# Optimization experiments

Measured on AMD Instinct MI355X. Metric: run time of the kernel, lower is better.

## Reference

```python
import math
import jax, jax.numpy as jnp
import numpy as np

WS = [2048, 4096, 8192]
RS = [1, 2, 4]
HEAD_IDX = 0


def build_indices(n):
    """Static dilated gather indices: concat of every segment's strided slice.

    Matches _prepare_sparse_indices for the chosen (ws, rs, n), which yields
    zero padding (each segment contributes exactly max_subatt_n indices).
    """
    max_m = min(n, max(w // r for w, r in zip(WS, RS)))
    parts = []
    for w, r in zip(WS, RS):
        offset = HEAD_IDX % r
        for s in range(0, n, w):
            seg = np.arange(s, min(s + w, n))[offset::r]
            assert len(seg) == max_m, "config chosen to avoid padding"
            parts.append(seg)
    return np.concatenate(parts).astype(np.int32), max_m


def _forward(x, Wq, Wk, Wv):
    b, n, c = x.shape
    idx_np, m = build_indices(n)
    idx = jnp.asarray(idx_np)            # [S], S = num_subatt * m
    S = idx_np.shape[0]
    nb = S // m                          # number of sub-attention windows

    # gather -> [b, S, c] -> batched windows [b*nb, m, c]
    bx = x[:, idx, :].reshape(b * nb, m, c)

    # single-head causal attention on each window, also return softmax denoms
    scale = 1.0 / math.sqrt(c)
    q = bx @ Wq
    k = bx @ Wk
    v = bx @ Wv
    logits = jnp.einsum('bqc,bkc->bqk', q, k) * scale
    causal = jnp.tril(jnp.ones((m, m), dtype=bool))
    logits = jnp.where(causal, logits, -jnp.inf)
    lse = jax.scipy.special.logsumexp(logits, axis=-1)   # [b*nb, m]
    probs = jnp.exp(logits - lse[..., None])
    o = jnp.einsum('bqk,bkc->bqc', probs, v)             # [b*nb, m, c]
    denoms = jnp.exp(lse)                                 # softmax denominators

    o = o.reshape(b, S, c)
    denoms = denoms.reshape(b, S)

    # _mix_outputs: scatter-add denoms per target position, reweight, scatter-add outputs
    denom_sums = jnp.zeros((b, n), x.dtype).at[:, idx].add(denoms)
    alphas = denoms / denom_sums[:, idx]                  # [b, S]
    out = jnp.zeros((b, n, c), x.dtype).at[:, idx, :].add(o * alphas[..., None])
    return out


def setup_inputs() -> dict:
    key = jax.random.key(0)
    kx, kq, kk, kv = jax.random.split(key, 4)
    b, n, c = 4, 8192, 64
    s = 1.0 / math.sqrt(c)
    return {
        'x': jax.random.normal(kx, (b, n, c), dtype=jnp.float32),
        'Wq': jax.random.normal(kq, (c, c), dtype=jnp.float32) * s,
        'Wk': jax.random.normal(kk, (c, c), dtype=jnp.float32) * s,
        'Wv': jax.random.normal(kv, (c, c), dtype=jnp.float32) * s,
    }


def reference(x, Wq, Wk, Wv):
    return _forward(x, Wq, Wk, Wv)
```

## Files before the change

kernel.cpp:

```cpp
#include <hip/hip_runtime.h>
#include <math.h>

#define NB   4
#define NSEQ 8192
#define CDIM 64
#define M    2048
#define NW   7
#define NBLK2 40

typedef _Float16 half8 __attribute__((ext_vector_type(8)));
typedef __fp16 fp16x2 __attribute__((ext_vector_type(2)));
typedef float f32x4 __attribute__((ext_vector_type(4)));
typedef unsigned short u16x4 __attribute__((ext_vector_type(4)));

#if defined(__has_builtin) && __has_builtin(__builtin_amdgcn_exp2f)
#define EXP2(x) __builtin_amdgcn_exp2f(x)
#else
#define EXP2(x) __expf((x) * 0.69314718056f)
#endif

#define QSCALE 0.1803368801111204f
#define PBIAS 4.0f

#define K_OFF   0
#define VT_OFF  8192
#define PS_OFF  16384

__device__ __forceinline__ int win_base(int w) {
    return (w < 4) ? (w << 11) : ((w < 6) ? ((w - 4) << 12) : 0);
}
__device__ __forceinline__ int win_stride(int w) {
    return (w < 4) ? 1 : ((w < 6) ? 2 : 4);
}

__global__ __launch_bounds__(256, 1) void qkv_proj(
        const float* __restrict__ x,
        const float* __restrict__ Wq, const float* __restrict__ Wk,
        const float* __restrict__ Wv,
        _Float16* __restrict__ Qg, _Float16* __restrict__ Kg,
        _Float16* __restrict__ Vg) {
    const int t = threadIdx.x;
    const int wid = t >> 6, lane = t & 63, l15 = lane & 15, quad = lane >> 4;

    half8 wb[3][2][4];
#pragma unroll
    for (int m = 0; m < 3; ++m) {
        const float* Wm = (m == 0) ? Wq : ((m == 1) ? Wk : Wv);
        const float sc = (m == 0) ? QSCALE : 1.0f;
#pragma unroll
        for (int kh = 0; kh < 2; ++kh)
#pragma unroll
            for (int nt = 0; nt < 4; ++nt) {
                float f[8];
#pragma unroll
                for (int j = 0; j < 8; ++j)
                    f[j] = Wm[(kh * 32 + quad * 8 + j) * 64 + nt * 16 + l15] * sc;
                union { fp16x2 h[4]; half8 v; } u;
#pragma unroll
                for (int p = 0; p < 4; ++p)
                    u.h[p] = __builtin_amdgcn_cvt_pkrtz(f[2 * p], f[2 * p + 1]);
                wb[m][kh][nt] = u.v;
            }
    }

    const int rowbase = blockIdx.x * 128 + wid * 32;
#pragma unroll
    for (int mt = 0; mt < 2; ++mt) {
        const int r0 = rowbase + mt * 16;
        half8 xa[2];
#pragma unroll
        for (int kh = 0; kh < 2; ++kh) {
            const float* xr = x + (size_t)(r0 + l15) * 64 + kh * 32 + quad * 8;
            const float4 a = *(const float4*)xr;
            const float4 b2 = *(const float4*)(xr + 4);
            union { fp16x2 h[4]; half8 v; } u;
            u.h[0] = __builtin_amdgcn_cvt_pkrtz(a.x, a.y);
            u.h[1] = __builtin_amdgcn_cvt_pkrtz(a.z, a.w);
            u.h[2] = __builtin_amdgcn_cvt_pkrtz(b2.x, b2.y);
            u.h[3] = __builtin_amdgcn_cvt_pkrtz(b2.z, b2.w);
            xa[kh] = u.v;
        }
#pragma unroll
        for (int m = 0; m < 3; ++m) {
            f32x4 acc[4];
#pragma unroll
            for (int nt = 0; nt < 4; ++nt) {
                acc[nt] = (f32x4){0.f, 0.f, 0.f, 0.f};
                acc[nt] = __builtin_amdgcn_mfma_f32_16x16x32_f16(xa[0], wb[m][0][nt], acc[nt], 0, 0, 0);
                acc[nt] = __builtin_amdgcn_mfma_f32_16x16x32_f16(xa[1], wb[m][1][nt], acc[nt], 0, 0, 0);
            }
            _Float16* outp = (m == 0) ? Qg : ((m == 1) ? Kg : Vg);
#pragma unroll
            for (int nt = 0; nt < 4; ++nt)
#pragma unroll
                for (int j = 0; j < 4; ++j)
                    outp[(size_t)(r0 + quad * 4 + j) * 64 + nt * 16 + l15] =
                        (_Float16)acc[nt][j];
        }
    }
}

__global__ __launch_bounds__(256, 4) void attn(
        const _Float16* __restrict__ Qg, const _Float16* __restrict__ Kg,
        const _Float16* __restrict__ Vg,
        _Float16* __restrict__ Op, float* __restrict__ LSEp) {
    __shared__ __align__(16) char smem[20480];

    int id = 39 - (int)blockIdx.x;
    int QT, ci;
    if (id < 4)       { QT = id;              ci = 0; }
    else if (id < 12) { int r = id - 4;  QT = 4  + (r >> 1); ci = r & 1; }
    else if (id < 24) { int r = id - 12; int q3 = r / 3; QT = 8 + q3; ci = r - 3 * q3; }
    else              { int r = id - 24; QT = 12 + (r >> 2); ci = r & 3; }
    const int w = blockIdx.y, b = blockIdx.z;
    const int base = win_base(w), stride = win_stride(w);
    const int g = QT >> 2;
    const int cb = 2 * g * (g + 1) + (QT & 3) * (g + 1);
    const int outblk = (b * NW + w) * NBLK2 + cb + ci;
    const int kt0 = ci * 16;
    const int ktmax = 4 * QT + 4;
    const int kt1 = (kt0 + 16 < ktmax) ? kt0 + 16 : ktmax;

    const _Float16* Qb = Qg + (size_t)b * NSEQ * 64;
    const _Float16* Kb = Kg + (size_t)b * NSEQ * 64;
    const _Float16* Vb = Vg + (size_t)b * NSEQ * 64;

    const int t = threadIdx.x;
    const int wid = t >> 6, lane = t & 63, l15 = lane & 15, quad = lane >> 4;

    const int sr = t >> 3, sch = t & 7;
    const int c4 = t & 15, kq = t >> 4;
    const int vd0 = 4 * c4;

    const size_t qr0 = (size_t)(base + stride * (QT * 128 + 16 * wid + l15)) * 64;
    const size_t qr1 = (size_t)(base + stride * (QT * 128 + 64 + 16 * wid + l15)) * 64;
    const half8 qa00 = *(const half8*)(Qb + qr0 + quad * 8);
    const half8 qa01 = *(const half8*)(Qb + qr0 + 32 + quad * 8);
    const half8 qa10 = *(const half8*)(Qb + qr1 + quad * 8);
    const half8 qa11 = *(const half8*)(Qb + qr1 + 32 + quad * 8);

    f32x4 oacc0[4], oacc1[4];
    float l_[8];
#pragma unroll
    for (int ns = 0; ns < 4; ++ns) {
        oacc0[ns] = (f32x4){0.f, 0.f, 0.f, 0.f};
        oacc1[ns] = (f32x4){0.f, 0.f, 0.f, 0.f};
    }
#pragma unroll
    for (int j = 0; j < 8; ++j) l_[j] = 0.f;

    half8 pk;
    u16x4 pv0, pv1;

    {
        const size_t ka = (size_t)(base + stride * (kt0 * 32 + sr)) * 64 + sch * 8;
        pk = *(const half8*)(Kb + ka);
        const size_t va = (size_t)(base + stride * (kt0 * 32 + kq)) * 64 + vd0;
        pv0 = *(const u16x4*)(Vb + va);
        pv1 = *(const u16x4*)(Vb + va + (size_t)stride * 16 * 64);
        char* Kd = smem + K_OFF;
        char* Vd = smem + VT_OFF;
        *(half8*)(Kd + sr * 128 + ((sch ^ (sr & 7)) * 16)) = pk;
#pragma unroll
        for (int i = 0; i < 4; ++i) {
            int d = vd0 + i;
            unsigned int pkw = (unsigned int)pv0[i] | ((unsigned int)pv1[i] << 16);
            int ch = ((kq >> 2) ^ (d & 3) ^ ((d >> 2) & 3)) & 3;
            *(unsigned int*)(Vd + d * 64 + ch * 16 + (kq & 3) * 4) = pkw;
        }
    }

    int cur = 0;
    for (int kt = kt0; kt < kt1; ++kt) {
        __syncthreads();
        const bool pf = (kt + 1 < kt1);
        if (pf) {
            const size_t ka = (size_t)(base + stride * ((kt + 1) * 32 + sr)) * 64 + sch * 8;
            pk = *(const half8*)(Kb + ka);
            const size_t va = (size_t)(base + stride * ((kt + 1) * 32 + kq)) * 64 + vd0;
            pv0 = *(const u16x4*)(Vb + va);
            pv1 = *(const u16x4*)(Vb + va + (size_t)stride * 16 * 64);
        }

        const char* Kd = smem + K_OFF + cur * 4096;
        const char* Vd = smem + VT_OFF + cur * 4096;
        char* PsB = smem + PS_OFF;

        half8 kb[2][2];
#pragma unroll
        for (int ns = 0; ns < 2; ++ns) {
            const int krow = ns * 16 + l15, swk = krow & 7;
            kb[ns][0] = *(const half8*)(Kd + krow * 128 + ((quad ^ swk) * 16));
            kb[ns][1] = *(const half8*)(Kd + krow * 128 + (((quad + 4) ^ swk) * 16));
        }
        f32x4 sa0[2], sa1[2];
#pragma unroll
        for (int ns = 0; ns < 2; ++ns) {
            f32x4 c0 = (f32x4){0.f, 0.f, 0.f, 0.f};
            c0 = __builtin_amdgcn_mfma_f32_16x16x32_f16(qa00, kb[ns][0], c0, 0, 0, 0);
            c0 = __builtin_amdgcn_mfma_f32_16x16x32_f16(qa01, kb[ns][1], c0, 0, 0, 0);
            sa0[ns] = c0;
            f32x4 c1 = (f32x4){0.f, 0.f, 0.f, 0.f};
            c1 = __builtin_amdgcn_mfma_f32_16x16x32_f16(qa10, kb[ns][0], c1, 0, 0, 0);
            c1 = __builtin_amdgcn_mfma_f32_16x16x32_f16(qa11, kb[ns][1], c1, 0, 0, 0);
            sa1[ns] = c1;
        }
        if (kt >= 4 * QT) {
            const int colb = kt * 32 + l15;
            const int row0 = QT * 128 + 16 * wid + quad * 4;
#pragma unroll
            for (int ns = 0; ns < 2; ++ns)
#pragma unroll
                for (int j = 0; j < 4; ++j) {
                    if (colb + ns * 16 > row0 + j)      sa0[ns][j] = -1e30f;
                    if (colb + ns * 16 > row0 + 64 + j) sa1[ns][j] = -1e30f;
                }
        }

        half8 vb[4];
#pragma unroll
        for (int ns = 0; ns < 4; ++ns) {
            const int d = ns * 16 + l15;
            const int ch = (quad ^ (d & 3) ^ ((d >> 2) & 3)) & 3;
            vb[ns] = *(const half8*)(Vd + d * 64 + ch * 16);
        }

#pragma unroll
        for (int j = 0; j < 4; ++j) {
            const int q = 16 * wid + quad * 4 + j;
            float p0 = EXP2(sa0[0][j] - PBIAS);
            float p1 = EXP2(sa0[1][j] - PBIAS);
            l_[j] += p0 + p1;
            union { fp16x2 h; unsigned int u; } pw;
            pw.h = __builtin_amdgcn_cvt_pkrtz(p0, p1);
            const int ch = ((l15 >> 2) ^ (q & 3) ^ ((q >> 2) & 3)) & 3;
            *(unsigned int*)(PsB + q * 64 + ch * 16 + (l15 & 3) * 4) = pw.u;
        }
        {
            const int qp = 16 * wid + l15;
            const int ch = (quad ^ (qp & 3) ^ ((qp >> 2) & 3)) & 3;
            half8 pa = *(const half8*)(PsB + qp * 64 + ch * 16);
#pragma unroll
            for (int ns = 0; ns < 4; ++ns)
                oacc0[ns] = __builtin_amdgcn_mfma_f32_16x16x32_f16(pa, vb[ns], oacc0[ns], 0, 0, 0);
        }

#pragma unroll
        for (int j = 0; j < 4; ++j) {
            const int q = 16 * wid + quad * 4 + j;
            float p0 = EXP2(sa1[0][j] - PBIAS);
            float p1 = EXP2(sa1[1][j] - PBIAS);
            l_[4 + j] += p0 + p1;
            union { fp16x2 h; unsigned int u; } pw;
            pw.h = __builtin_amdgcn_cvt_pkrtz(p0, p1);
            const int ch = ((l15 >> 2) ^ (q & 3) ^ ((q >> 2) & 3)) & 3;
            *(unsigned int*)(PsB + q * 64 + ch * 16 + (l15 & 3) * 4) = pw.u;
        }
        {
            const int qp = 16 * wid + l15;
            const int ch = (quad ^ (qp & 3) ^ ((qp >> 2) & 3)) & 3;
            half8 pa = *(const half8*)(PsB + qp * 64 + ch * 16);
#pragma unroll
            for (int ns = 0; ns < 4; ++ns)
                oacc1[ns] = __builtin_amdgcn_mfma_f32_16x16x32_f16(pa, vb[ns], oacc1[ns], 0, 0, 0);
        }

        if (pf) {
            char* Kn = smem + K_OFF + (cur ^ 1) * 4096;
            char* Vn = smem + VT_OFF + (cur ^ 1) * 4096;
            *(half8*)(Kn + sr * 128 + ((sch ^ (sr & 7)) * 16)) = pk;
#pragma unroll
            for (int i = 0; i < 4; ++i) {
                int d = vd0 + i;
                unsigned int pkw = (unsigned int)pv0[i] | ((unsigned int)pv1[i] << 16);
                int ch = ((kq >> 2) ^ (d & 3) ^ ((d >> 2) & 3)) & 3;
                *(unsigned int*)(Vn + d * 64 + ch * 16 + (kq & 3) * 4) = pkw;
            }
        }
        cur ^= 1;
    }

#pragma unroll
    for (int j = 0; j < 8; ++j) {
        float s = l_[j];
        s += __shfl_xor(s, 1, 16);
        s += __shfl_xor(s, 2, 16);
        s += __shfl_xor(s, 4, 16);
        s += __shfl_xor(s, 8, 16);
        l_[j] = s;
    }
    const int qrow0 = 16 * wid + quad * 4;
    if (l15 == 0) {
#pragma unroll
        for (int j = 0; j < 4; ++j) {
            LSEp[(size_t)outblk * 128 + qrow0 + j]      = __logf(l_[j]);
            LSEp[(size_t)outblk * 128 + 64 + qrow0 + j] = __logf(l_[4 + j]);
        }
    }
#pragma unroll
    for (int j = 0; j < 4; ++j) {
        const float inv0 = 1.0f / l_[j];
        const float inv1 = 1.0f / l_[4 + j];
        const size_t r0off = ((size_t)outblk * 128 + qrow0 + j) * 64 + l15;
        const size_t r1off = ((size_t)outblk * 128 + 64 + qrow0 + j) * 64 + l15;
#pragma unroll
        for (int ns = 0; ns < 4; ++ns) {
            Op[r0off + ns * 16] = (_Float16)(oacc0[ns][j] * inv0);
            Op[r1off + ns * 16] = (_Float16)(oacc1[ns][j] * inv1);
        }
    }
}

typedef _Float16 half8v __attribute__((ext_vector_type(8)));
__global__ __launch_bounds__(256) void mix_out(
        const _Float16* __restrict__ Op, const float* __restrict__ LSEp,
        float* __restrict__ out) {
    int gid = blockIdx.x * 256 + threadIdx.x;
    int f8 = gid & 7;
    int tpos = (gid >> 3) & (NSEQ - 1);
    int b = gid >> 16;

    int idxs[12];
    float lse[12];
    int nref = 0;
    {
        int w = tpos >> 11, j = tpos & (M - 1);
        int QT = j >> 7, gg = QT >> 2, q = j & 127;
        int cbase = 2 * gg * (gg + 1) + (QT & 3) * (gg + 1);
        int bb = ((b * NW + w) * NBLK2 + cbase) * 128 + q;
        int cmax = j >> 9;
        for (int c = 0; c <= cmax; ++c) { idxs[nref] = bb + c * 128; lse[nref] = LSEp[idxs[nref]]; ++nref; }
    }
    if (!(tpos & 1)) {
        int w = 4 + (tpos >> 12), j = (tpos & 4095) >> 1;
        int QT = j >> 7, gg = QT >> 2, q = j & 127;
        int cbase = 2 * gg * (gg + 1) + (QT & 3) * (gg + 1);
        int bb = ((b * NW + w) * NBLK2 + cbase) * 128 + q;
        int cmax = j >> 9;
        for (int c = 0; c <= cmax; ++c) { idxs[nref] = bb + c * 128; lse[nref] = LSEp[idxs[nref]]; ++nref; }
    }
    if (!(tpos & 3)) {
        int j = tpos >> 2;
        int QT = j >> 7, gg = QT >> 2, q = j & 127;
        int cbase = 2 * gg * (gg + 1) + (QT & 3) * (gg + 1);
        int bb = ((b * NW + 6) * NBLK2 + cbase) * 128 + q;
        int cmax = j >> 9;
        for (int c = 0; c <= cmax; ++c) { idxs[nref] = bb + c * 128; lse[nref] = LSEp[idxs[nref]]; ++nref; }
    }

    float Mx = -1e30f;
    for (int i = 0; i < nref; ++i) Mx = fmaxf(Mx, lse[i]);
    float acc[8];
#pragma unroll
    for (int k = 0; k < 8; ++k) acc[k] = 0.f;
    float wsum = 0.f;
    for (int i = 0; i < nref; ++i) {
        float a = __expf(lse[i] - Mx);
        wsum += a;
        half8v v = *(const half8v*)(Op + (size_t)idxs[i] * 64 + f8 * 8);
#pragma unroll
        for (int k = 0; k < 8; ++k) acc[k] += a * (float)v[k];
    }
    float inv = 1.0f / wsum;
    size_t o = ((size_t)b * NSEQ + tpos) * 64 + f8 * 8;
    float4 r0 = make_float4(acc[0] * inv, acc[1] * inv, acc[2] * inv, acc[3] * inv);
    float4 r1 = make_float4(acc[4] * inv, acc[5] * inv, acc[6] * inv, acc[7] * inv);
    *(float4*)&out[o] = r0;
    *(float4*)&out[o + 4] = r1;
}

extern "C" void kernel_launch(void* const* d_in, const int* in_sizes, int n_in,
                              void* d_out, int out_size, void* d_ws, size_t ws_size,
                              hipStream_t stream) {
    const float* x  = (const float*)d_in[0];
    const float* Wq = (const float*)d_in[1];
    const float* Wk = (const float*)d_in[2];
    const float* Wv = (const float*)d_in[3];
    float* out = (float*)d_out;

    const size_t QN = (size_t)NB * NSEQ * CDIM;
    _Float16* Qg = (_Float16*)d_ws;
    _Float16* Kg = Qg + QN;
    _Float16* Vg = Kg + QN;
    _Float16* Op = Vg + QN;
    float* LSEp  = (float*)(Op + (size_t)NB * NW * NBLK2 * 128 * 64);

    qkv_proj<<<NB * NSEQ / 128, 256, 0, stream>>>(x, Wq, Wk, Wv, Qg, Kg, Vg);
    attn<<<dim3(NBLK2, NW, NB), 256, 0, stream>>>(Qg, Kg, Vg, Op, LSEp);
    mix_out<<<(NB * NSEQ * 8) / 256, 256, 0, stream>>>(Op, LSEp, out);
}
```

Measured before the change: 122.5 us.

## Double P scratch buffers, raise MFMA wave priority, and unroll mix_out gathers

The attention kernel now writes both halves of the probability tile into separate LDS buffers, so the two P·V MFMA groups issue back to back instead of alternating with softmax work. MFMA sections are wrapped in s_setprio so matrix work is scheduled ahead of other waves' instructions. mix_out replaces its variable-length loops with fixed 12-slot unrolled loads, masking inactive slots with -1e30, so all gathers can be in flight at once. The costs are 4 KB more LDS per block, redundant loads for masked slots, and more registers in mix_out.

Result: no change. 123.5 us (+0.8%).

```diff
diff --git a/kernel.cpp b/kernel.cpp
--- a/kernel.cpp
+++ b/kernel.cpp
@@ -24,7 +24,8 @@
 
 #define K_OFF   0
 #define VT_OFF  8192
-#define PS_OFF  16384
+#define PS0_OFF 16384
+#define PS1_OFF 20480
 
 __device__ __forceinline__ int win_base(int w) {
     return (w < 4) ? (w << 11) : ((w < 6) ? ((w - 4) << 12) : 0);
@@ -104,7 +105,7 @@
         const _Float16* __restrict__ Qg, const _Float16* __restrict__ Kg,
         const _Float16* __restrict__ Vg,
         _Float16* __restrict__ Op, float* __restrict__ LSEp) {
-    __shared__ __align__(16) char smem[20480];
+    __shared__ __align__(16) char smem[24576];
 
     int id = 39 - (int)blockIdx.x;
     int QT, ci;
@@ -184,7 +185,8 @@
 
         const char* Kd = smem + K_OFF + cur * 4096;
         const char* Vd = smem + VT_OFF + cur * 4096;
-        char* PsB = smem + PS_OFF;
+        char* Ps0 = smem + PS0_OFF;
+        char* Ps1 = smem + PS1_OFF;
 
         half8 kb[2][2];
 #pragma unroll
@@ -194,6 +196,7 @@
             kb[ns][1] = *(const half8*)(Kd + krow * 128 + (((quad + 4) ^ swk) * 16));
         }
         f32x4 sa0[2], sa1[2];
+        __builtin_amdgcn_s_setprio(1);
 #pragma unroll
         for (int ns = 0; ns < 2; ++ns) {
             f32x4 c0 = (f32x4){0.f, 0.f, 0.f, 0.f};
@@ -205,6 +208,7 @@
             c1 = __builtin_amdgcn_mfma_f32_16x16x32_f16(qa11, kb[ns][1], c1, 0, 0, 0);
             sa1[ns] = c1;
         }
+        __builtin_amdgcn_s_setprio(0);
         if (kt >= 4 * QT) {
             const int colb = kt * 32 + l15;
             const int row0 = QT * 128 + 16 * wid + quad * 4;
@@ -234,17 +238,8 @@
             union { fp16x2 h; unsigned int u; } pw;
             pw.h = __builtin_amdgcn_cvt_pkrtz(p0, p1);
             const int ch = ((l15 >> 2) ^ (q & 3) ^ ((q >> 2) & 3)) & 3;
-            *(unsigned int*)(PsB + q * 64 + ch * 16 + (l15 & 3) * 4) = pw.u;
-        }
-        {
-            const int qp = 16 * wid + l15;
-            const int ch = (quad ^ (qp & 3) ^ ((qp >> 2) & 3)) & 3;
-            half8 pa = *(const half8*)(PsB + qp * 64 + ch * 16);
-#pragma unroll
-            for (int ns = 0; ns < 4; ++ns)
-                oacc0[ns] = __builtin_amdgcn_mfma_f32_16x16x32_f16(pa, vb[ns], oacc0[ns], 0, 0, 0);
-        }
-
+            *(unsigned int*)(Ps0 + q * 64 + ch * 16 + (l15 & 3) * 4) = pw.u;
+        }
 #pragma unroll
         for (int j = 0; j < 4; ++j) {
             const int q = 16 * wid + quad * 4 + j;
@@ -254,15 +249,21 @@
             union { fp16x2 h; unsigned int u; } pw;
             pw.h = __builtin_amdgcn_cvt_pkrtz(p0, p1);
             const int ch = ((l15 >> 2) ^ (q & 3) ^ ((q >> 2) & 3)) & 3;
-            *(unsigned int*)(PsB + q * 64 + ch * 16 + (l15 & 3) * 4) = pw.u;
+            *(unsigned int*)(Ps1 + q * 64 + ch * 16 + (l15 & 3) * 4) = pw.u;
         }
         {
             const int qp = 16 * wid + l15;
             const int ch = (quad ^ (qp & 3) ^ ((qp >> 2) & 3)) & 3;
-            half8 pa = *(const half8*)(PsB + qp * 64 + ch * 16);
+            half8 pa0 = *(const half8*)(Ps0 + qp * 64 + ch * 16);
+            half8 pa1 = *(const half8*)(Ps1 + qp * 64 + ch * 16);
+            __builtin_amdgcn_s_setprio(1);
 #pragma unroll
             for (int ns = 0; ns < 4; ++ns)
-                oacc1[ns] = __builtin_amdgcn_mfma_f32_16x16x32_f16(pa, vb[ns], oacc1[ns], 0, 0, 0);
+                oacc0[ns] = __builtin_amdgcn_mfma_f32_16x16x32_f16(pa0, vb[ns], oacc0[ns], 0, 0, 0);
+#pragma unroll
+            for (int ns = 0; ns < 4; ++ns)
+                oacc1[ns] = __builtin_amdgcn_mfma_f32_16x16x32_f16(pa1, vb[ns], oacc1[ns], 0, 0, 0);
+            __builtin_amdgcn_s_setprio(0);
         }
 
         if (pf) {
@@ -320,46 +321,73 @@
     int tpos = (gid >> 3) & (NSEQ - 1);
     int b = gid >> 16;
 
-    int idxs[12];
+    int idx[12];
     float lse[12];
-    int nref = 0;
+
     {
         int w = tpos >> 11, j = tpos & (M - 1);
         int QT = j >> 7, gg = QT >> 2, q = j & 127;
         int cbase = 2 * gg * (gg + 1) + (QT & 3) * (gg + 1);
         int bb = ((b * NW + w) * NBLK2 + cbase) * 128 + q;
         int cmax = j >> 9;
-        for (int c = 0; c <= cmax; ++c) { idxs[nref] = bb + c * 128; lse[nref] = LSEp[idxs[nref]]; ++nref; }
-    }
-    if (!(tpos & 1)) {
+#pragma unroll
+        for (int c = 0; c < 4; ++c) {
+            int cc = (c <= cmax) ? c : cmax;
+            idx[c] = bb + cc * 128;
+            float v = LSEp[idx[c]];
+            lse[c] = (c <= cmax) ? v : -1e30f;
+        }
+    }
+    {
+        int act = ((tpos & 1) == 0);
         int w = 4 + (tpos >> 12), j = (tpos & 4095) >> 1;
         int QT = j >> 7, gg = QT >> 2, q = j & 127;
         int cbase = 2 * gg * (gg + 1) + (QT & 3) * (gg + 1);
         int bb = ((b * NW + w) * NBLK2 + cbase) * 128 + q;
         int cmax = j >> 9;
-        for (int c = 0; c <= cmax; ++c) { idxs[nref] = bb + c * 128; lse[nref] = LSEp[idxs[nref]]; ++nref; }
-    }
-    if (!(tpos & 3)) {
+#pragma unroll
+        for (int c = 0; c < 4; ++c) {
+            int cc = (c <= cmax) ? c : cmax;
+            idx[4 + c] = bb + cc * 128;
+            float v = LSEp[idx[4 + c]];
+            lse[4 + c] = (act && c <= cmax) ? v : -1e30f;
+        }
+    }
+    {
+        int act = ((tpos & 3) == 0);
         int j = tpos >> 2;
         int QT = j >> 7, gg = QT >> 2, q = j & 127;
         int cbase = 2 * gg * (gg + 1) + (QT & 3) * (gg + 1);
         int bb = ((b * NW + 6) * NBLK2 + cbase) * 128 + q;
         int cmax = j >> 9;
-        for (int c = 0; c <= cmax; ++c) { idxs[nref] = bb + c * 128; lse[nref] = LSEp[idxs[nref]]; ++nref; }
-    }
+#pragma unroll
+        for (int c = 0; c < 4; ++c) {
+            int cc = (c <= cmax) ? c : cmax;
+            idx[8 + c] = bb + cc * 128;
+            float v = LSEp[idx[8 + c]];
+            lse[8 + c] = (act && c <= cmax) ? v : -1e30f;
+        }
+    }
+
+    half8v v[12];
+#pragma unroll
+    for (int i = 0; i < 12; ++i)
+        v[i] = *(const half8v*)(Op + (size_t)idx[i] * 64 + f8 * 8);
 
     float Mx = -1e30f;
-    for (int i = 0; i < nref; ++i) Mx = fmaxf(Mx, lse[i]);
+#pragma unroll
+    for (int i = 0; i < 12; ++i) Mx = fmaxf(Mx, lse[i]);
+
     float acc[8];
 #pragma unroll
     for (int k = 0; k < 8; ++k) acc[k] = 0.f;
     float wsum = 0.f;
-    for (int i = 0; i < nref; ++i) {
+#pragma unroll
+    for (int i = 0; i < 12; ++i) {
         float a = __expf(lse[i] - Mx);
         wsum += a;
-        half8v v = *(const half8v*)(Op + (size_t)idxs[i] * 64 + f8 * 8);
-#pragma unroll
-        for (int k = 0; k < 8; ++k) acc[k] += a * (float)v[k];
+#pragma unroll
+        for (int k = 0; k < 8; ++k) acc[k] += a * (float)v[i][k];
     }
     float inv = 1.0f / wsum;
     size_t o = ((size_t)b * NSEQ + tpos) * 64 + f8 * 8;
```
